# Performance work log

Measured on AMD Instinct MI355X. Metric: run time of the kernel, lower is better.

## Reference

```python
import jax, jax.numpy as jnp
import numpy as np

N = 1024
H = 128


def setup_inputs() -> dict:
    key = jax.random.key(0)
    ks = jax.random.split(key, 12)
    s = 0.05
    inp = {
        "h": jax.random.normal(ks[0], (N, H), dtype=jnp.float32),
        "x": jax.random.normal(ks[1], (N, 2), dtype=jnp.float32),
        "batch": jnp.zeros((N,), dtype=jnp.int32),
        # attention projections (torch Linear: y = x @ W.T + b)
        "Wq": jax.random.normal(ks[2], (H, H), dtype=jnp.float32) * s,
        "bq": jnp.zeros((H,), dtype=jnp.float32),
        "Wk": jax.random.normal(ks[3], (H, H), dtype=jnp.float32) * s,
        "bk": jnp.zeros((H,), dtype=jnp.float32),
        "Wv": jax.random.normal(ks[4], (H, H), dtype=jnp.float32) * s,
        "bv": jnp.zeros((H,), dtype=jnp.float32),
        # edge_mlp: Linear(2,H) -> ReLU -> Linear(H,H)
        "We1": jax.random.normal(ks[5], (H, 2), dtype=jnp.float32) * s,
        "be1": jnp.zeros((H,), dtype=jnp.float32),
        "We2": jax.random.normal(ks[6], (H, H), dtype=jnp.float32) * s,
        "be2": jnp.zeros((H,), dtype=jnp.float32),
        # coord_mlp: Linear(H,1)
        "Wc": jax.random.normal(ks[7], (1, H), dtype=jnp.float32) * s,
        "bc": jnp.zeros((1,), dtype=jnp.float32),
    }
    return inp


def reference(h, x, batch, Wq, bq, Wk, bk, Wv, bv, We1, be1, We2, be2, Wc, bc):
    # rel_x[i, j] = x[i] - x[j]  -> [N, N, 2]
    rel_x = x[:, None, :] - x[None, :, :]
    # edge MLP over all pairs -> [N, N, H]
    edge_feat = jax.nn.relu(rel_x @ We1.T + be1) @ We2.T + be2
    q = h @ Wq.T + bq  # [N, H]
    k = h @ Wk.T + bk
    v = h @ Wv.T + bv
    scale = 1.0 / np.sqrt(float(H)).astype(np.float32)
    attn = jax.nn.softmax((q @ k.T) * scale, axis=-1)  # [N, N]
    agg_h = attn @ v  # [N, H]
    coord_w = edge_feat @ Wc.T + bc  # [N, N, 1]
    # weighted coordinate diffusion, summed over neighbors j (axis=1)
    delta_x = jnp.sum(attn[:, :, None] * (coord_w * rel_x), axis=1)  # [N, 2]
    return (h + agg_h, x + delta_x)
```

## Files before the change

kernel.cpp:

```cpp
#include <hip/hip_runtime.h>
#include <hip/hip_fp16.h>

#define NN 1024
#define HH 128
#define QR 2
#define TPB 1024

typedef _Float16 f16x2_t __attribute__((ext_vector_type(2)));

__device__ __forceinline__ float dot2(__half2 a, __half2 b, float c) {
#if __has_builtin(__builtin_amdgcn_fdot2)
  return __builtin_amdgcn_fdot2(__builtin_bit_cast(f16x2_t, a),
                                __builtin_bit_cast(f16x2_t, b), c, false);
#else
  return fmaf(__low2float(a), __low2float(b),
              fmaf(__high2float(a), __high2float(b), c));
#endif
}

__device__ __forceinline__ __half2 relu2(__half2 a) {
#if __has_builtin(__builtin_elementwise_max)
  f16x2_t v = __builtin_bit_cast(f16x2_t, a);
  f16x2_t z = {(_Float16)0.f, (_Float16)0.f};
  return __builtin_bit_cast(__half2, __builtin_elementwise_max(v, z));
#else
  unsigned int av = __builtin_bit_cast(unsigned int, a);
  unsigned int rv;
  asm("v_pk_max_f16 %0, %1, 0" : "=v"(rv) : "v"(av));
  return __builtin_bit_cast(__half2, rv);
#endif
}

__device__ __forceinline__ float2 wmax2(float2 v) {
#pragma unroll
  for (int off = 1; off < 64; off <<= 1) {
    v.x = fmaxf(v.x, __shfl_xor(v.x, off));
    v.y = fmaxf(v.y, __shfl_xor(v.y, off));
  }
  return v;
}
__device__ __forceinline__ float2 wsum2(float2 v) {
#pragma unroll
  for (int off = 1; off < 64; off <<= 1) {
    v.x += __shfl_xor(v.x, off);
    v.y += __shfl_xor(v.y, off);
  }
  return v;
}

__global__ __launch_bounds__(128)
void prep_kernel(const float* __restrict__ Wq, const float* __restrict__ Wk,
                 const float* __restrict__ Wv, const float* __restrict__ We1,
                 const float* __restrict__ be1, const float* __restrict__ We2,
                 const float* __restrict__ be2, const float* __restrict__ Wc,
                 const float* __restrict__ bc,
                 float* __restrict__ WqT, float* __restrict__ WkT,
                 float* __restrict__ WvT, float* __restrict__ epack,
                 float* __restrict__ c0,
                 __half2* __restrict__ aB, __half2* __restrict__ bB,
                 __half2* __restrict__ uB) {
  __shared__ float su[HH];
  const int d = blockIdx.x;
  const int o = threadIdx.x;
  WqT[d * HH + o] = Wq[o * HH + d];
  WkT[d * HH + o] = Wk[o * HH + d];
  WvT[d * HH + o] = Wv[o * HH + d];
  if (d == 0) {
    float uu = 0.f;
    for (int e = 0; e < HH; ++e) uu = fmaf(Wc[e], We2[e * HH + o], uu);
    su[o] = uu;
    epack[o * 4 + 0] = We1[2 * o];
    epack[o * 4 + 1] = We1[2 * o + 1];
    epack[o * 4 + 2] = be1[o];
    epack[o * 4 + 3] = uu;
    if (o == 0) {
      float s = bc[0];
      for (int e = 0; e < HH; ++e) s = fmaf(Wc[e], be2[e], s);
      c0[0] = s;
    }
    __syncthreads();
    if (o < 64) {
      aB[o] = __halves2half2(__float2half(We1[4 * o]), __float2half(We1[4 * o + 2]));
      bB[o] = __halves2half2(__float2half(We1[4 * o + 1]), __float2half(We1[4 * o + 3]));
      uB[o] = __halves2half2(__float2half(su[2 * o]), __float2half(su[2 * o + 1]));
    }
  }
}

__global__ __launch_bounds__(128)
void qkv_kernel(const float* __restrict__ hin,
                const float* __restrict__ WqT, const float* __restrict__ WkT,
                const float* __restrict__ WvT,
                const float* __restrict__ bq, const float* __restrict__ bk,
                const float* __restrict__ bv,
                __half* __restrict__ q16, __half* __restrict__ kP,
                __half* __restrict__ v16) {
  __shared__ __align__(16) float hT[HH][QR];
  const int tid = threadIdx.x;
  const int i0 = blockIdx.x * QR;
#pragma unroll
  for (int r = 0; r < QR; ++r) hT[tid][r] = hin[(i0 + r) * HH + tid];
  __syncthreads();
  float qa0 = 0.f, qa1 = 0.f, ka0 = 0.f, ka1 = 0.f, va0 = 0.f, va1 = 0.f;
#pragma unroll 4
  for (int d = 0; d < HH; ++d) {
    float wq = WqT[d * HH + tid];
    float wk = WkT[d * HH + tid];
    float wv = WvT[d * HH + tid];
    float2 hh = *(const float2*)&hT[d][0];
    qa0 = fmaf(hh.x, wq, qa0); qa1 = fmaf(hh.y, wq, qa1);
    ka0 = fmaf(hh.x, wk, ka0); ka1 = fmaf(hh.y, wk, ka1);
    va0 = fmaf(hh.x, wv, va0); va1 = fmaf(hh.y, wv, va1);
  }
  const float scale = 0.08838834764831845f;
  float bqv = bq[tid], bkv = bk[tid], bvv = bv[tid];
  q16[(i0 + 0) * HH + tid] = __float2half((qa0 + bqv) * scale);
  q16[(i0 + 1) * HH + tid] = __float2half((qa1 + bqv) * scale);
  v16[(i0 + 0) * HH + tid] = __float2half(va0 + bvv);
  v16[(i0 + 1) * HH + tid] = __float2half(va1 + bvv);
  float kb0 = ka0 + bkv, kb1 = ka1 + bkv;
  float pr0 = __shfl_xor(kb0, 1);
  float pr1 = __shfl_xor(kb1, 1);
  if ((tid & 1) == 0) {
    const int dp = tid >> 1;
    __half2 w0 = __halves2half2(__float2half(kb0), __float2half(pr0));
    __half2 w1 = __halves2half2(__float2half(kb1), __float2half(pr1));
    *(__half2*)&kP[dp * (2 * NN) + 2 * i0]     = w0;
    *(__half2*)&kP[dp * (2 * NN) + 2 * i0 + 2] = w1;
  }
}

__global__ __launch_bounds__(TPB, 8)
void fused_kernel(const __half* __restrict__ q16, const __half* __restrict__ kP,
                  const __half* __restrict__ v16, const float* __restrict__ hin,
                  const float* __restrict__ x, const float* __restrict__ epack,
                  const __half2* __restrict__ aB, const __half2* __restrict__ bB,
                  const __half2* __restrict__ uB, const float* __restrict__ c0p,
                  float* __restrict__ out_h, float* __restrict__ out_x) {
  __shared__ __align__(16) float spA[NN];
  __shared__ __align__(16) float spB[NN];
  __shared__ __align__(16) float4 sredh[16][64];
  __shared__ __half2 stabA[64];
  __shared__ __half2 stabB[64];
  __shared__ float2 sredm[16], sreds[16], sredx[16], sredy[16];

  const int tid = threadIdx.x;
  const int lane = tid & 63;
  const int wid = tid >> 6;
  const int i0 = blockIdx.x * 2;
  const int j = tid;

  if (tid < 64) {
    const float4 ea = ((const float4*)epack)[2 * tid];
    const float4 eb = ((const float4*)epack)[2 * tid + 1];
    float x0x = x[i0 * 2 + 0], x0y = x[i0 * 2 + 1];
    float x1x = x[i0 * 2 + 2], x1y = x[i0 * 2 + 3];
    stabA[tid] = __halves2half2(
        __float2half(fmaf(ea.x, x0x, fmaf(ea.y, x0y, ea.z))),
        __float2half(fmaf(eb.x, x0x, fmaf(eb.y, x0y, eb.z))));
    stabB[tid] = __halves2half2(
        __float2half(fmaf(ea.x, x1x, fmaf(ea.y, x1y, ea.z))),
        __float2half(fmaf(eb.x, x1x, fmaf(eb.y, x1y, eb.z))));
  }

  const __half2* q0p = (const __half2*)(q16 + (i0 + 0) * HH);
  const __half2* q1p = (const __half2*)(q16 + (i0 + 1) * HH);
  float s0 = 0.f, s1 = 0.f;
#pragma unroll 8
  for (int dp = 0; dp < HH / 2; ++dp) {
    __half2 kk = *(const __half2*)&kP[dp * (2 * NN) + 2 * j];
    s0 = dot2(kk, q0p[dp], s0);
    s1 = dot2(kk, q1p[dp], s1);
  }

  float2 mv = wmax2(make_float2(s0, s1));
  if (lane == 0) sredm[wid] = mv;
  __syncthreads();
  float2 mm = sredm[0];
#pragma unroll
  for (int w2 = 1; w2 < 16; ++w2) {
    float2 t2 = sredm[w2];
    mm.x = fmaxf(mm.x, t2.x); mm.y = fmaxf(mm.y, t2.y);
  }

  float e0 = __expf(s0 - mm.x), e1 = __expf(s1 - mm.y);
  spA[j] = e0; spB[j] = e1;
  float2 sv = wsum2(make_float2(e0, e1));
  if (lane == 0) sreds[wid] = sv;
  __syncthreads();
  float2 ssv = sreds[0];
#pragma unroll
  for (int w2 = 1; w2 < 16; ++w2) { ssv.x += sreds[w2].x; ssv.y += sreds[w2].y; }
  const float inv0 = 1.f / ssv.x, inv1 = 1.f / ssv.y;

  {
    const int op = tid & 63;
    const int c = tid >> 6;
    float hA0 = 0.f, hB0 = 0.f, hA1 = 0.f, hB1 = 0.f;
#pragma unroll 4
    for (int jj = 0; jj < NN / 16; ++jj) {
      int jv = c * (NN / 16) + jj;
      __half2 vv = *(const __half2*)&v16[jv * HH + 2 * op];
      float vx = __low2float(vv), vy = __high2float(vv);
      float p0 = spA[jv];
      float p1 = spB[jv];
      hA0 = fmaf(p0, vx, hA0); hB0 = fmaf(p0, vy, hB0);
      hA1 = fmaf(p1, vx, hA1); hB1 = fmaf(p1, vy, hB1);
    }
    sredh[c][op] = make_float4(hA0, hB0, hA1, hB1);
  }

  float2 xj = *(const float2*)&x[2 * j];
  __half2 xjx2 = __float2half2_rn(xj.x);
  __half2 xjy2 = __float2half2_rn(xj.y);
  float wa0 = 0.f, wa1 = 0.f;
#pragma unroll 8
  for (int tp = 0; tp < 64; ++tp) {
    __half2 a2 = aB[tp], b2 = bB[tp], u2 = uB[tp];
    __half2 w2 = __hfma2(a2, xjx2, __hmul2(b2, xjy2));
    wa0 = dot2(u2, relu2(__hsub2(stabA[tp], w2)), wa0);
    wa1 = dot2(u2, relu2(__hsub2(stabB[tp], w2)), wa1);
  }
  const float c0v = c0p[0];
  float cw0 = e0 * (wa0 + c0v);
  float cw1 = e1 * (wa1 + c0v);
  float xi0x = x[i0 * 2 + 0], xi0y = x[i0 * 2 + 1];
  float xi1x = x[i0 * 2 + 2], xi1y = x[i0 * 2 + 3];
  float2 rx = wsum2(make_float2(cw0 * (xi0x - xj.x), cw1 * (xi1x - xj.x)));
  float2 ry = wsum2(make_float2(cw0 * (xi0y - xj.y), cw1 * (xi1y - xj.y)));
  if (lane == 0) { sredx[wid] = rx; sredy[wid] = ry; }

  __syncthreads();

  if (tid < 2 * HH) {
    const int r = tid >> 7, o = tid & 127;
    float hv = 0.f;
#pragma unroll
    for (int c2 = 0; c2 < 16; ++c2)
      hv += ((const float*)&sredh[c2][o >> 1])[(r << 1) | (o & 1)];
    float invr = r ? inv1 : inv0;
    out_h[(i0 + r) * HH + o] = hin[(i0 + r) * HH + o] + hv * invr;
  }
  if (tid < 2) {
    float sx = 0.f, sy = 0.f;
#pragma unroll
    for (int w2 = 0; w2 < 16; ++w2) {
      sx += tid ? sredx[w2].y : sredx[w2].x;
      sy += tid ? sredy[w2].y : sredy[w2].x;
    }
    float invr = tid ? inv1 : inv0;
    out_x[(i0 + tid) * 2 + 0] = x[(i0 + tid) * 2 + 0] + sx * invr;
    out_x[(i0 + tid) * 2 + 1] = x[(i0 + tid) * 2 + 1] + sy * invr;
  }
}

extern "C" void kernel_launch(void* const* d_in, const int* in_sizes, int n_in,
                              void* d_out, int out_size, void* d_ws, size_t ws_size,
                              hipStream_t stream) {
  (void)in_sizes; (void)n_in; (void)out_size; (void)ws_size;
  const float* h   = (const float*)d_in[0];
  const float* x   = (const float*)d_in[1];
  const float* Wq  = (const float*)d_in[3];
  const float* bq  = (const float*)d_in[4];
  const float* Wk  = (const float*)d_in[5];
  const float* bk  = (const float*)d_in[6];
  const float* Wv  = (const float*)d_in[7];
  const float* bv  = (const float*)d_in[8];
  const float* We1 = (const float*)d_in[9];
  const float* be1 = (const float*)d_in[10];
  const float* We2 = (const float*)d_in[11];
  const float* be2 = (const float*)d_in[12];
  const float* Wc  = (const float*)d_in[13];
  const float* bc  = (const float*)d_in[14];

  float* ws   = (float*)d_ws;
  float* WqT  = ws;
  float* WkT  = WqT + HH * HH;
  float* WvT  = WkT + HH * HH;
  float* ep   = WvT + HH * HH;
  float* c0   = ep + 4 * HH;
  __half* q16 = (__half*)(c0 + 8);
  __half* kP  = q16 + NN * HH;
  __half* v16 = kP + NN * HH;
  __half2* aB = (__half2*)(v16 + NN * HH);
  __half2* bB = aB + 64;
  __half2* uB = bB + 64;

  float* out_h = (float*)d_out;
  float* out_x = out_h + NN * HH;

  prep_kernel<<<dim3(HH), dim3(128), 0, stream>>>(
      Wq, Wk, Wv, We1, be1, We2, be2, Wc, bc, WqT, WkT, WvT, ep, c0, aB, bB, uB);
  qkv_kernel<<<dim3(NN / QR), dim3(128), 0, stream>>>(
      h, WqT, WkT, WvT, bq, bk, bv, q16, kP, v16);
  fused_kernel<<<dim3(NN / 2), dim3(TPB), 0, stream>>>(
      q16, kP, v16, h, x, ep, aB, bB, uB, c0, out_h, out_x);
}
```

Baseline: 135.9 us.

## Split attention over key chunks with 8-row tiles and a separate softmax-merge kernel

Replaces the single fused kernel (2 query rows per 1024-thread block, all 1024 keys) with a split-K scheme. Each 512-thread block handles 8 query rows against 128 keys and writes partial max, sum, coordinate and PV results to workspace. A second kernel merges them flash-decoding style. K is re-laid out into 8-half chunks so each thread reads 16-byte vectors, and each V element loaded now serves 8 rows instead of 2. The cost is extra workspace traffic and a third launch.

```diff
diff --git a/kernel.cpp b/kernel.cpp
--- a/kernel.cpp
+++ b/kernel.cpp
@@ -4,7 +4,10 @@
 #define NN 1024
 #define HH 128
 #define QR 2
-#define TPB 1024
+#define ITR 8
+#define JS 8
+#define JT (NN/JS)
+#define TPA 512
 
 typedef _Float16 f16x2_t __attribute__((ext_vector_type(2)));
 
@@ -93,7 +96,7 @@
                 const float* __restrict__ WvT,
                 const float* __restrict__ bq, const float* __restrict__ bk,
                 const float* __restrict__ bv,
-                __half* __restrict__ q16, __half* __restrict__ kP,
+                __half* __restrict__ q16, __half* __restrict__ k8,
                 __half* __restrict__ v16) {
   __shared__ __align__(16) float hT[HH][QR];
   const int tid = threadIdx.x;
@@ -116,141 +119,204 @@
   float bqv = bq[tid], bkv = bk[tid], bvv = bv[tid];
   q16[(i0 + 0) * HH + tid] = __float2half((qa0 + bqv) * scale);
   q16[(i0 + 1) * HH + tid] = __float2half((qa1 + bqv) * scale);
+  const int c = tid >> 3, slot = tid & 7;
+  k8[(size_t)((c * NN + i0 + 0) << 3) + slot] = __float2half(ka0 + bkv);
+  k8[(size_t)((c * NN + i0 + 1) << 3) + slot] = __float2half(ka1 + bkv);
   v16[(i0 + 0) * HH + tid] = __float2half(va0 + bvv);
   v16[(i0 + 1) * HH + tid] = __float2half(va1 + bvv);
-  float kb0 = ka0 + bkv, kb1 = ka1 + bkv;
-  float pr0 = __shfl_xor(kb0, 1);
-  float pr1 = __shfl_xor(kb1, 1);
-  if ((tid & 1) == 0) {
-    const int dp = tid >> 1;
-    __half2 w0 = __halves2half2(__float2half(kb0), __float2half(pr0));
-    __half2 w1 = __halves2half2(__float2half(kb1), __float2half(pr1));
-    *(__half2*)&kP[dp * (2 * NN) + 2 * i0]     = w0;
-    *(__half2*)&kP[dp * (2 * NN) + 2 * i0 + 2] = w1;
-  }
-}
-
-__global__ __launch_bounds__(TPB, 8)
-void fused_kernel(const __half* __restrict__ q16, const __half* __restrict__ kP,
-                  const __half* __restrict__ v16, const float* __restrict__ hin,
-                  const float* __restrict__ x, const float* __restrict__ epack,
-                  const __half2* __restrict__ aB, const __half2* __restrict__ bB,
-                  const __half2* __restrict__ uB, const float* __restrict__ c0p,
-                  float* __restrict__ out_h, float* __restrict__ out_x) {
-  __shared__ __align__(16) float spA[NN];
-  __shared__ __align__(16) float spB[NN];
-  __shared__ __align__(16) float4 sredh[16][64];
-  __shared__ __half2 stabA[64];
-  __shared__ __half2 stabB[64];
-  __shared__ float2 sredm[16], sreds[16], sredx[16], sredy[16];
+}
+
+__global__ __launch_bounds__(TPA, 8)
+void stageA_kernel(const __half* __restrict__ q16, const __half* __restrict__ k8,
+                   const __half* __restrict__ v16, const float* __restrict__ x,
+                   const float* __restrict__ epack,
+                   const __half2* __restrict__ aB, const __half2* __restrict__ bB,
+                   const __half2* __restrict__ uB, const float* __restrict__ c0p,
+                   float2* __restrict__ ws_sm, float2* __restrict__ ws_cxy,
+                   float* __restrict__ ws_pv) {
+  __shared__ __align__(16) float sp[JT][ITR];
+  __shared__ __align__(16) float sred[ITR][8][HH];
+  __shared__ __half2 stab[ITR][64];
+  __shared__ float2 redm[8], reds[8], redx[8], redy[8];
 
   const int tid = threadIdx.x;
   const int lane = tid & 63;
   const int wid = tid >> 6;
-  const int i0 = blockIdx.x * 2;
-  const int j = tid;
-
-  if (tid < 64) {
-    const float4 ea = ((const float4*)epack)[2 * tid];
-    const float4 eb = ((const float4*)epack)[2 * tid + 1];
-    float x0x = x[i0 * 2 + 0], x0y = x[i0 * 2 + 1];
-    float x1x = x[i0 * 2 + 2], x1y = x[i0 * 2 + 3];
-    stabA[tid] = __halves2half2(
-        __float2half(fmaf(ea.x, x0x, fmaf(ea.y, x0y, ea.z))),
-        __float2half(fmaf(eb.x, x0x, fmaf(eb.y, x0y, eb.z))));
-    stabB[tid] = __halves2half2(
-        __float2half(fmaf(ea.x, x1x, fmaf(ea.y, x1y, ea.z))),
-        __float2half(fmaf(eb.x, x1x, fmaf(eb.y, x1y, eb.z))));
-  }
-
-  const __half2* q0p = (const __half2*)(q16 + (i0 + 0) * HH);
-  const __half2* q1p = (const __half2*)(q16 + (i0 + 1) * HH);
+  const int b = blockIdx.x;
+  const int it = b >> 3, js = b & 7;
+  const int i0 = it * ITR;
+  const int jb = js * JT;
+
+  {
+    const int r = tid & 7, tp = tid >> 3;
+    const float4 ea = ((const float4*)epack)[2 * tp];
+    const float4 eb = ((const float4*)epack)[2 * tp + 1];
+    float xrx = x[(i0 + r) * 2 + 0], xry = x[(i0 + r) * 2 + 1];
+    stab[r][tp] = __halves2half2(
+        __float2half(fmaf(ea.x, xrx, fmaf(ea.y, xry, ea.z))),
+        __float2half(fmaf(eb.x, xrx, fmaf(eb.y, xry, eb.z))));
+  }
+
+  const int jl = tid & (JT - 1);
+  const int rg = tid >> 7;
+  const int jg = jb + jl;
+
+  const __half2* q0p = (const __half2*)(q16 + (size_t)(i0 + 2 * rg) * HH);
+  const __half2* q1p = (const __half2*)(q16 + (size_t)(i0 + 2 * rg + 1) * HH);
+  const float4* k84 = (const float4*)k8;
   float s0 = 0.f, s1 = 0.f;
-#pragma unroll 8
-  for (int dp = 0; dp < HH / 2; ++dp) {
-    __half2 kk = *(const __half2*)&kP[dp * (2 * NN) + 2 * j];
-    s0 = dot2(kk, q0p[dp], s0);
-    s1 = dot2(kk, q1p[dp], s1);
+#pragma unroll
+  for (int c = 0; c < 16; ++c) {
+    float4 ka = k84[c * NN + jg];
+    __half2 a0 = __builtin_bit_cast(__half2, ka.x);
+    __half2 a1 = __builtin_bit_cast(__half2, ka.y);
+    __half2 a2 = __builtin_bit_cast(__half2, ka.z);
+    __half2 a3 = __builtin_bit_cast(__half2, ka.w);
+    __half2 qa0 = q0p[4 * c + 0], qa1 = q0p[4 * c + 1];
+    __half2 qa2 = q0p[4 * c + 2], qa3 = q0p[4 * c + 3];
+    __half2 qb0 = q1p[4 * c + 0], qb1 = q1p[4 * c + 1];
+    __half2 qb2 = q1p[4 * c + 2], qb3 = q1p[4 * c + 3];
+    s0 = dot2(a0, qa0, s0); s0 = dot2(a1, qa1, s0);
+    s0 = dot2(a2, qa2, s0); s0 = dot2(a3, qa3, s0);
+    s1 = dot2(a0, qb0, s1); s1 = dot2(a1, qb1, s1);
+    s1 = dot2(a2, qb2, s1); s1 = dot2(a3, qb3, s1);
   }
 
   float2 mv = wmax2(make_float2(s0, s1));
-  if (lane == 0) sredm[wid] = mv;
+  if (lane == 0) redm[wid] = mv;
   __syncthreads();
-  float2 mm = sredm[0];
-#pragma unroll
-  for (int w2 = 1; w2 < 16; ++w2) {
-    float2 t2 = sredm[w2];
-    mm.x = fmaxf(mm.x, t2.x); mm.y = fmaxf(mm.y, t2.y);
-  }
-
-  float e0 = __expf(s0 - mm.x), e1 = __expf(s1 - mm.y);
-  spA[j] = e0; spB[j] = e1;
+  float2 ma = redm[2 * rg], mb = redm[2 * rg + 1];
+  float mmx = fmaxf(ma.x, mb.x), mmy = fmaxf(ma.y, mb.y);
+  float e0 = __expf(s0 - mmx), e1 = __expf(s1 - mmy);
+  sp[jl][2 * rg] = e0; sp[jl][2 * rg + 1] = e1;
   float2 sv = wsum2(make_float2(e0, e1));
-  if (lane == 0) sreds[wid] = sv;
-  __syncthreads();
-  float2 ssv = sreds[0];
-#pragma unroll
-  for (int w2 = 1; w2 < 16; ++w2) { ssv.x += sreds[w2].x; ssv.y += sreds[w2].y; }
-  const float inv0 = 1.f / ssv.x, inv1 = 1.f / ssv.y;
-
-  {
-    const int op = tid & 63;
-    const int c = tid >> 6;
-    float hA0 = 0.f, hB0 = 0.f, hA1 = 0.f, hB1 = 0.f;
-#pragma unroll 4
-    for (int jj = 0; jj < NN / 16; ++jj) {
-      int jv = c * (NN / 16) + jj;
-      __half2 vv = *(const __half2*)&v16[jv * HH + 2 * op];
-      float vx = __low2float(vv), vy = __high2float(vv);
-      float p0 = spA[jv];
-      float p1 = spB[jv];
-      hA0 = fmaf(p0, vx, hA0); hB0 = fmaf(p0, vy, hB0);
-      hA1 = fmaf(p1, vx, hA1); hB1 = fmaf(p1, vy, hB1);
-    }
-    sredh[c][op] = make_float4(hA0, hB0, hA1, hB1);
-  }
-
-  float2 xj = *(const float2*)&x[2 * j];
+  if (lane == 0) reds[wid] = sv;
+
+  float2 xj = *(const float2*)&x[2 * jg];
   __half2 xjx2 = __float2half2_rn(xj.x);
   __half2 xjy2 = __float2half2_rn(xj.y);
   float wa0 = 0.f, wa1 = 0.f;
 #pragma unroll 8
   for (int tp = 0; tp < 64; ++tp) {
     __half2 a2 = aB[tp], b2 = bB[tp], u2 = uB[tp];
-    __half2 w2 = __hfma2(a2, xjx2, __hmul2(b2, xjy2));
-    wa0 = dot2(u2, relu2(__hsub2(stabA[tp], w2)), wa0);
-    wa1 = dot2(u2, relu2(__hsub2(stabB[tp], w2)), wa1);
+    __half2 w2h = __hfma2(a2, xjx2, __hmul2(b2, xjy2));
+    wa0 = dot2(u2, relu2(__hsub2(stab[2 * rg][tp], w2h)), wa0);
+    wa1 = dot2(u2, relu2(__hsub2(stab[2 * rg + 1][tp], w2h)), wa1);
   }
   const float c0v = c0p[0];
   float cw0 = e0 * (wa0 + c0v);
   float cw1 = e1 * (wa1 + c0v);
-  float xi0x = x[i0 * 2 + 0], xi0y = x[i0 * 2 + 1];
-  float xi1x = x[i0 * 2 + 2], xi1y = x[i0 * 2 + 3];
+  float xi0x = x[(i0 + 2 * rg) * 2 + 0],     xi0y = x[(i0 + 2 * rg) * 2 + 1];
+  float xi1x = x[(i0 + 2 * rg + 1) * 2 + 0], xi1y = x[(i0 + 2 * rg + 1) * 2 + 1];
   float2 rx = wsum2(make_float2(cw0 * (xi0x - xj.x), cw1 * (xi1x - xj.x)));
   float2 ry = wsum2(make_float2(cw0 * (xi0y - xj.y), cw1 * (xi1y - xj.y)));
-  if (lane == 0) { sredx[wid] = rx; sredy[wid] = ry; }
-
+  if (lane == 0) { redx[wid] = rx; redy[wid] = ry; }
   __syncthreads();
 
-  if (tid < 2 * HH) {
-    const int r = tid >> 7, o = tid & 127;
-    float hv = 0.f;
-#pragma unroll
-    for (int c2 = 0; c2 < 16; ++c2)
-      hv += ((const float*)&sredh[c2][o >> 1])[(r << 1) | (o & 1)];
-    float invr = r ? inv1 : inv0;
-    out_h[(i0 + r) * HH + o] = hin[(i0 + r) * HH + o] + hv * invr;
-  }
-  if (tid < 2) {
-    float sx = 0.f, sy = 0.f;
-#pragma unroll
-    for (int w2 = 0; w2 < 16; ++w2) {
-      sx += tid ? sredx[w2].y : sredx[w2].x;
-      sy += tid ? sredy[w2].y : sredy[w2].x;
-    }
-    float invr = tid ? inv1 : inv0;
-    out_x[(i0 + tid) * 2 + 0] = x[(i0 + tid) * 2 + 0] + sx * invr;
-    out_x[(i0 + tid) * 2 + 1] = x[(i0 + tid) * 2 + 1] + sy * invr;
+  if (tid < ITR) {
+    const int r = tid, g = r >> 1;
+    float2 sa = reds[2 * g], sb = reds[2 * g + 1];
+    float2 m2a = redm[2 * g], m2b = redm[2 * g + 1];
+    float2 xa = redx[2 * g], xb = redx[2 * g + 1];
+    float2 ya = redy[2 * g], yb = redy[2 * g + 1];
+    float sum, mrow, cx, cy;
+    if (r & 1) { sum = sa.y + sb.y; mrow = fmaxf(m2a.y, m2b.y); cx = xa.y + xb.y; cy = ya.y + yb.y; }
+    else       { sum = sa.x + sb.x; mrow = fmaxf(m2a.x, m2b.x); cx = xa.x + xb.x; cy = ya.x + yb.x; }
+    ws_sm[b * ITR + r]  = make_float2(sum, mrow);
+    ws_cxy[b * ITR + r] = make_float2(cx, cy);
+  }
+
+  {
+    const int fp = tid & 63;
+    const int cc = tid >> 6;
+    const __half2* v2 = (const __half2*)v16;
+    float accA[8], accB[8];
+#pragma unroll
+    for (int r = 0; r < 8; ++r) { accA[r] = 0.f; accB[r] = 0.f; }
+#pragma unroll 4
+    for (int jj = 0; jj < 16; ++jj) {
+      const int jl2 = cc * 16 + jj;
+      __half2 vv = v2[(size_t)(jb + jl2) * 64 + fp];
+      float vx = __low2float(vv), vy = __high2float(vv);
+      const float4* pr = (const float4*)&sp[jl2][0];
+      float4 pa = pr[0], pb = pr[1];
+      accA[0] = fmaf(pa.x, vx, accA[0]); accB[0] = fmaf(pa.x, vy, accB[0]);
+      accA[1] = fmaf(pa.y, vx, accA[1]); accB[1] = fmaf(pa.y, vy, accB[1]);
+      accA[2] = fmaf(pa.z, vx, accA[2]); accB[2] = fmaf(pa.z, vy, accB[2]);
+      accA[3] = fmaf(pa.w, vx, accA[3]); accB[3] = fmaf(pa.w, vy, accB[3]);
+      accA[4] = fmaf(pb.x, vx, accA[4]); accB[4] = fmaf(pb.x, vy, accB[4]);
+      accA[5] = fmaf(pb.y, vx, accA[5]); accB[5] = fmaf(pb.y, vy, accB[5]);
+      accA[6] = fmaf(pb.z, vx, accA[6]); accB[6] = fmaf(pb.z, vy, accB[6]);
+      accA[7] = fmaf(pb.w, vx, accA[7]); accB[7] = fmaf(pb.w, vy, accB[7]);
+    }
+#pragma unroll
+    for (int r = 0; r < 8; ++r)
+      *(float2*)&sred[r][cc][2 * fp] = make_float2(accA[r], accB[r]);
+  }
+  __syncthreads();
+
+  {
+    const int f = tid & 127, rp = tid >> 7;
+    float a0 = 0.f, a1 = 0.f;
+#pragma unroll
+    for (int c2 = 0; c2 < 8; ++c2) {
+      a0 += sred[2 * rp][c2][f];
+      a1 += sred[2 * rp + 1][c2][f];
+    }
+    ws_pv[(size_t)(b * ITR + 2 * rp) * HH + f]     = a0;
+    ws_pv[(size_t)(b * ITR + 2 * rp + 1) * HH + f] = a1;
+  }
+}
+
+__global__ __launch_bounds__(1024)
+void stageB_kernel(const float2* __restrict__ ws_sm, const float2* __restrict__ ws_cxy,
+                   const float* __restrict__ ws_pv, const float* __restrict__ hin,
+                   const float* __restrict__ x,
+                   float* __restrict__ out_h, float* __restrict__ out_x) {
+  const int it = blockIdx.x;
+  const int tid = threadIdx.x;
+  const int f = tid & 127, r = tid >> 7;
+  const int i0 = it * ITR;
+
+  float m[JS], s[JS];
+  float M = -1e30f;
+#pragma unroll
+  for (int js = 0; js < JS; ++js) {
+    float2 sm = ws_sm[(it * JS + js) * ITR + r];
+    s[js] = sm.x; m[js] = sm.y; M = fmaxf(M, sm.y);
+  }
+  float sc[JS], S = 0.f;
+#pragma unroll
+  for (int js = 0; js < JS; ++js) { sc[js] = __expf(m[js] - M); S = fmaf(sc[js], s[js], S); }
+  const float inv = 1.f / S;
+
+  float acc = 0.f;
+#pragma unroll
+  for (int js = 0; js < JS; ++js)
+    acc = fmaf(sc[js], ws_pv[(size_t)((it * JS + js) * ITR + r) * HH + f], acc);
+  out_h[(i0 + r) * HH + f] = hin[(i0 + r) * HH + f] + acc * inv;
+
+  if (tid < ITR) {
+    const int rr = tid;
+    float mm2[JS], ss2[JS];
+    float MM = -1e30f;
+#pragma unroll
+    for (int js = 0; js < JS; ++js) {
+      float2 sm = ws_sm[(it * JS + js) * ITR + rr];
+      ss2[js] = sm.x; mm2[js] = sm.y; MM = fmaxf(MM, sm.y);
+    }
+    float SS = 0.f, cx = 0.f, cy = 0.f;
+#pragma unroll
+    for (int js = 0; js < JS; ++js) {
+      float scj = __expf(mm2[js] - MM);
+      SS = fmaf(scj, ss2[js], SS);
+      float2 c2 = ws_cxy[(it * JS + js) * ITR + rr];
+      cx = fmaf(scj, c2.x, cx);
+      cy = fmaf(scj, c2.y, cy);
+    }
+    float invr = 1.f / SS;
+    out_x[(i0 + rr) * 2 + 0] = x[(i0 + rr) * 2 + 0] + cx * invr;
+    out_x[(i0 + rr) * 2 + 1] = x[(i0 + rr) * 2 + 1] + cy * invr;
   }
 }
 
@@ -280,11 +346,14 @@
   float* ep   = WvT + HH * HH;
   float* c0   = ep + 4 * HH;
   __half* q16 = (__half*)(c0 + 8);
-  __half* kP  = q16 + NN * HH;
-  __half* v16 = kP + NN * HH;
+  __half* k8  = q16 + NN * HH;
+  __half* v16 = k8 + NN * HH;
   __half2* aB = (__half2*)(v16 + NN * HH);
   __half2* bB = aB + 64;
   __half2* uB = bB + 64;
+  float2* ws_sm  = (float2*)(uB + 64);
+  float2* ws_cxy = ws_sm + (128 * JS * ITR);
+  float*  ws_pv  = (float*)(ws_cxy + (128 * JS * ITR));
 
   float* out_h = (float*)d_out;
   float* out_x = out_h + NN * HH;
@@ -292,7 +361,9 @@
   prep_kernel<<<dim3(HH), dim3(128), 0, stream>>>(
       Wq, Wk, Wv, We1, be1, We2, be2, Wc, bc, WqT, WkT, WvT, ep, c0, aB, bB, uB);
   qkv_kernel<<<dim3(NN / QR), dim3(128), 0, stream>>>(
-      h, WqT, WkT, WvT, bq, bk, bv, q16, kP, v16);
-  fused_kernel<<<dim3(NN / 2), dim3(TPB), 0, stream>>>(
-      q16, kP, v16, h, x, ep, aB, bB, uB, c0, out_h, out_x);
-}
+      h, WqT, WkT, WvT, bq, bk, bv, q16, k8, v16);
+  stageA_kernel<<<dim3(128 * JS), dim3(TPA), 0, stream>>>(
+      q16, k8, v16, x, ep, aB, bB, uB, c0, ws_sm, ws_cxy, ws_pv);
+  stageB_kernel<<<dim3(128), dim3(1024), 0, stream>>>(
+      ws_sm, ws_cxy, ws_pv, h, x, out_h, out_x);
+}
```

After: 128.0 us. -5.9%, faster.
